# Kernel tuning notes

Hardware: AMD Instinct MI355X
Metric: run time of the kernel (lower is better)

Reference implementation:

```python
import jax, jax.numpy as jnp
import numpy as np
from jax import lax

B, N, S = 4, 16384, 4096
D1, D2 = 128, 256
MLP = (256, 128)
EPS_W = 1e-8
EPS_BN = 1e-5
BIG = 1e8


def setup_inputs() -> dict:
    key = jax.random.key(0)
    ks = jax.random.split(key, 10)
    inp = {
        "xyz1": jax.random.normal(ks[0], (B, 3, N), jnp.float32),
        "xyz2": jax.random.normal(ks[1], (B, 3, S), jnp.float32),
        "points1": jax.random.normal(ks[2], (B, D1, N), jnp.float32),
        "points2": jax.random.normal(ks[3], (B, D2, S), jnp.float32),
        "idx1": jnp.repeat(jnp.arange(B, dtype=jnp.int32), N).reshape(B, N),
        "idx2": jnp.repeat(jnp.arange(B, dtype=jnp.int32), S).reshape(B, S),
    }
    cin = D1 + D2
    inp["w1"] = jax.random.normal(ks[4], (MLP[0], cin), jnp.float32) * 0.05
    inp["b1"] = jnp.zeros((MLP[0],), jnp.float32)
    inp["g1"] = jnp.ones((MLP[0],), jnp.float32)
    inp["be1"] = jnp.zeros((MLP[0],), jnp.float32)
    inp["w2"] = jax.random.normal(ks[5], (MLP[1], MLP[0]), jnp.float32) * 0.05
    inp["b2"] = jnp.zeros((MLP[1],), jnp.float32)
    inp["g2"] = jnp.ones((MLP[1],), jnp.float32)
    inp["be2"] = jnp.zeros((MLP[1],), jnp.float32)
    return inp


def _bn_relu(x, gamma, beta):
    # training-mode batchnorm over (B, N) per channel, then relu; x: [B, C, N]
    mean = jnp.mean(x, axis=(0, 2), keepdims=True)
    var = jnp.var(x, axis=(0, 2), keepdims=True)  # biased, as torch BN
    xn = (x - mean) * lax.rsqrt(var + EPS_BN)
    return jax.nn.relu(xn * gamma[None, :, None] + beta[None, :, None])


def _fp_forward(xyz1, xyz2, points1, points2, idx1, idx2,
                w1, b1, g1, be1, w2, b2, g2, be2):
    x1 = jnp.transpose(xyz1, (0, 2, 1))  # [B, N, 3]
    x2 = jnp.transpose(xyz2, (0, 2, 1))  # [B, S, 3]
    p2 = jnp.transpose(points2, (0, 2, 1))  # [B, S, D2]

    # squared pairwise distances [B, N, S]
    d = -2.0 * jnp.einsum('bnc,bsc->bns', x1, x2)
    d = d + jnp.sum(x1 * x1, -1)[:, :, None] + jnp.sum(x2 * x2, -1)[:, None, :]
    d = jnp.where(idx1[:, :, None] == idx2[:, None, :], d, jnp.inf)

    # 3 nearest neighbors (top-k on negated distances == sort-ascending take 3)
    neg_d3, idx3 = lax.top_k(-d, 3)          # [B, N, 3]
    d3 = -neg_d3
    recip = 1.0 / (d3 + EPS_W)
    weight = recip / jnp.sum(recip, axis=2, keepdims=True)
    weight = jnp.where(d3 > BIG, 0.0, weight)
    weight = jnp.nan_to_num(weight)

    gathered = jax.vmap(lambda p, i: p[i])(p2, idx3)   # [B, N, 3, D2]
    interp = jnp.sum(gathered * weight[..., None], axis=2)  # [B, N, D2]

    newp = jnp.concatenate([jnp.transpose(points1, (0, 2, 1)), interp], axis=-1)
    newp = jnp.transpose(newp, (0, 2, 1))  # [B, D1+D2, N]

    # 1x1 conv -> BN -> relu, twice
    h = jnp.einsum('bcn,oc->bon', newp, w1) + b1[None, :, None]
    h = _bn_relu(h, g1, be1)
    h = jnp.einsum('bcn,oc->bon', h, w2) + b2[None, :, None]
    h = _bn_relu(h, g2, be2)
    return h


def reference(xyz1, xyz2, points1, points2, idx1, idx2,
              w1, b1, g1, be1, w2, b2, g2, be2):
    return _fp_forward(xyz1, xyz2, points1, points2, idx1, idx2,
                       w1, b1, g1, be1, w2, b2, g2, be2)
```

## Files before the change

### kernel.cpp

```cpp
#include <hip/hip_runtime.h>
#include <hip/hip_bf16.h>

#define INF_F (__builtin_inff())

typedef __attribute__((ext_vector_type(8))) short bf16x8;
typedef __attribute__((ext_vector_type(4))) float f32x4;

__device__ __forceinline__ unsigned short f2bf(float f) {
  __hip_bfloat16 h = __float2bfloat16(f);
  return __builtin_bit_cast(unsigned short, h);
}
__device__ __forceinline__ float bf2f(unsigned short u) {
  return __uint_as_float((unsigned)u << 16);
}

#define TOP3_INS(d, sj, E0, E1, E2, J0, J1, J2)                      \
  {                                                                  \
    bool l0 = (d) < E0, l1 = (d) < E1;                               \
    E2 = l1 ? E1 : (d); J2 = l1 ? J1 : (sj);                         \
    E1 = l0 ? E0 : (l1 ? (d) : E1); J1 = l0 ? J0 : (l1 ? (sj) : J1); \
    E0 = l0 ? (d) : E0; J0 = l0 ? (sj) : J0;                         \
  }


__global__ __launch_bounds__(256) void transpose_k(const float* __restrict__ in,
                                                   unsigned short* __restrict__ out) {
  __shared__ float tile[32][33];
  int b = blockIdx.z;
  int s0 = blockIdx.x * 32;
  int k0 = blockIdx.y * 32;
  int tx = threadIdx.x, ty = threadIdx.y;
  const float* src = in + ((size_t)b * 256 + k0) * 4096 + s0;
  for (int r = ty; r < 32; r += 8) tile[r][tx] = src[(size_t)r * 4096 + tx];
  __syncthreads();
  unsigned short* dst = out + ((size_t)b * 4096 + s0) * 256 + k0;
  for (int r = ty; r < 32; r += 8) dst[(size_t)r * 256 + tx] = f2bf(tile[tx][r]);
}

__global__ __launch_bounds__(256) void p1t_k(const float* __restrict__ p1,
                                             unsigned short* __restrict__ X) {
  __shared__ float tile[32][33];
  int b = blockIdx.z;
  int n0 = blockIdx.x * 32;
  int c0 = blockIdx.y * 32;
  int tx = threadIdx.x, ty = threadIdx.y;
  const float* src = p1 + ((size_t)b * 128 + c0) * 16384 + n0;
  for (int r = ty; r < 32; r += 8) tile[r][tx] = src[(size_t)r * 16384 + tx];
  __syncthreads();
  for (int r = ty; r < 32; r += 8)
    X[((size_t)(b * 16384 + n0 + r)) * 384 + c0 + tx] = f2bf(tile[tx][r]);
}

__global__ __launch_bounds__(256) void wcvt_k(const float* __restrict__ w1,
                                              const float* __restrict__ w2,
                                              unsigned short* __restrict__ w1b,
                                              unsigned short* __restrict__ w2b) {
  int id = blockIdx.x * 256 + threadIdx.x;
  if (id < 98304) w1b[id] = f2bf(w1[id]);
  else w2b[id - 98304] = f2bf(w2[id - 98304]);
}

__global__ __launch_bounds__(256) void knn_k(const float* __restrict__ xyz1,
                                             const float* __restrict__ xyz2,
                                             const int* __restrict__ idx1,
                                             const int* __restrict__ idx2,
                                             float* __restrict__ rec) {
  __shared__ float4 sP[256];
  int bid = blockIdx.x;
  int chunk = bid >> 4, sl = bid & 15;
  int b = chunk >> 4;
  int nloc = (chunk & 15) << 10;
  int t = threadIdx.x;
  int common = idx1[b * 16384 + nloc];
  int sbase = sl << 8;
  {
    int gs = sbase + t;
    float x = xyz2[(b * 3 + 0) * 4096 + gs];
    float y = xyz2[(b * 3 + 1) * 4096 + gs];
    float z = xyz2[(b * 3 + 2) * 4096 + gs];
    float w = fmaf(x, x, fmaf(y, y, z * z));
    int sid = idx2[b * 4096 + gs];
    w = (sid == common) ? w : 3e38f;
    sP[t] = make_float4(x, y, z, w);
  }
  __syncthreads();
  int q0i = b * 16384 + nloc + t;
  float px0 = xyz1[(b * 3 + 0) * 16384 + nloc + t];
  float py0 = xyz1[(b * 3 + 1) * 16384 + nloc + t];
  float pz0 = xyz1[(b * 3 + 2) * 16384 + nloc + t];
  float px1 = xyz1[(b * 3 + 0) * 16384 + nloc + t + 256];
  float py1 = xyz1[(b * 3 + 1) * 16384 + nloc + t + 256];
  float pz1 = xyz1[(b * 3 + 2) * 16384 + nloc + t + 256];
  float px2 = xyz1[(b * 3 + 0) * 16384 + nloc + t + 512];
  float py2 = xyz1[(b * 3 + 1) * 16384 + nloc + t + 512];
  float pz2 = xyz1[(b * 3 + 2) * 16384 + nloc + t + 512];
  float px3 = xyz1[(b * 3 + 0) * 16384 + nloc + t + 768];
  float py3 = xyz1[(b * 3 + 1) * 16384 + nloc + t + 768];
  float pz3 = xyz1[(b * 3 + 2) * 16384 + nloc + t + 768];
  int id0 = idx1[q0i], id1 = idx1[q0i + 256], id2 = idx1[q0i + 512], id3 = idx1[q0i + 768];
  float pn0 = fmaf(px0, px0, fmaf(py0, py0, pz0 * pz0));
  float pn1 = fmaf(px1, px1, fmaf(py1, py1, pz1 * pz1));
  float pn2 = fmaf(px2, px2, fmaf(py2, py2, pz2 * pz2));
  float pn3 = fmaf(px3, px3, fmaf(py3, py3, pz3 * pz3));
  float e00 = INF_F, e10 = INF_F, e20 = INF_F;
  float e01 = INF_F, e11 = INF_F, e21 = INF_F;
  float e02 = INF_F, e12 = INF_F, e22 = INF_F;
  float e03 = INF_F, e13 = INF_F, e23 = INF_F;
  int j00 = 0, j10 = 0, j20 = 0;
  int j01 = 0, j11 = 0, j21 = 0;
  int j02 = 0, j12 = 0, j22 = 0;
  int j03 = 0, j13 = 0, j23 = 0;
#pragma unroll 2
  for (int s = 0; s < 256; ++s) {
    float4 p = sP[s];
    int sj = sbase + s;
    float d0 = fmaf(-2.f, fmaf(px0, p.x, fmaf(py0, p.y, pz0 * p.z)), pn0 + p.w);
    float d1 = fmaf(-2.f, fmaf(px1, p.x, fmaf(py1, p.y, pz1 * p.z)), pn1 + p.w);
    float d2 = fmaf(-2.f, fmaf(px2, p.x, fmaf(py2, p.y, pz2 * p.z)), pn2 + p.w);
    float d3 = fmaf(-2.f, fmaf(px3, p.x, fmaf(py3, p.y, pz3 * p.z)), pn3 + p.w);
    if (d0 < e20) TOP3_INS(d0, sj, e00, e10, e20, j00, j10, j20);
    if (d1 < e21) TOP3_INS(d1, sj, e01, e11, e21, j01, j11, j21);
    if (d2 < e22) TOP3_INS(d2, sj, e02, e12, e22, j02, j12, j22);
    if (d3 < e23) TOP3_INS(d3, sj, e03, e13, e23, j03, j13, j23);
  }
#define KNN_FB(MYID, PX, PY, PZ, PN, E0, E1, E2, J0, J1, J2)              \
  if (__builtin_expect((MYID) != common, 0)) {                            \
    E0 = INF_F; E1 = INF_F; E2 = INF_F; J0 = 0; J1 = 0; J2 = 0;           \
    for (int s = 0; s < 256; ++s) {                                       \
      int gs = sbase + s;                                                 \
      float x = xyz2[(b * 3 + 0) * 4096 + gs];                            \
      float y = xyz2[(b * 3 + 1) * 4096 + gs];                            \
      float z = xyz2[(b * 3 + 2) * 4096 + gs];                            \
      float w = fmaf(x, x, fmaf(y, y, z * z));                            \
      float d = fmaf(-2.f, fmaf(PX, x, fmaf(PY, y, (PZ) * z)), (PN) + w); \
      d = (idx2[b * 4096 + gs] == (MYID)) ? d : INF_F;                    \
      if (d < E2) TOP3_INS(d, gs, E0, E1, E2, J0, J1, J2);                \
    }                                                                     \
  }
  KNN_FB(id0, px0, py0, pz0, pn0, e00, e10, e20, j00, j10, j20);
  KNN_FB(id1, px1, py1, pz1, pn1, e01, e11, e21, j01, j11, j21);
  KNN_FB(id2, px2, py2, pz2, pn2, e02, e12, e22, j02, j12, j22);
  KNN_FB(id3, px3, py3, pz3, pn3, e03, e13, e23, j03, j13, j23);
#undef KNN_FB
  {
    float* r = &rec[((size_t)sl * 65536 + q0i) * 6];
    r[0] = e00; r[1] = e10; r[2] = e20;
    ((int*)r)[3] = j00; ((int*)r)[4] = j10; ((int*)r)[5] = j20;
    r = &rec[((size_t)sl * 65536 + q0i + 256) * 6];
    r[0] = e01; r[1] = e11; r[2] = e21;
    ((int*)r)[3] = j01; ((int*)r)[4] = j11; ((int*)r)[5] = j21;
    r = &rec[((size_t)sl * 65536 + q0i + 512) * 6];
    r[0] = e02; r[1] = e12; r[2] = e22;
    ((int*)r)[3] = j02; ((int*)r)[4] = j12; ((int*)r)[5] = j22;
    r = &rec[((size_t)sl * 65536 + q0i + 768) * 6];
    r[0] = e03; r[1] = e13; r[2] = e23;
    ((int*)r)[3] = j03; ((int*)r)[4] = j13; ((int*)r)[5] = j23;
  }
}

__global__ __launch_bounds__(256) void knnmerge_k(const float* __restrict__ rec,
                                                  int* __restrict__ idx3,
                                                  float* __restrict__ wgt) {
  int i = blockIdx.x * 256 + threadIdx.x;
  float e0, e1, e2;
  int j0, j1, j2;
  {
    const float* r = &rec[(size_t)i * 6];
    e0 = r[0]; e1 = r[1]; e2 = r[2];
    j0 = ((const int*)r)[3]; j1 = ((const int*)r)[4]; j2 = ((const int*)r)[5];
  }
  for (int c = 1; c < 16; ++c) {
    const float* r = &rec[((size_t)c * 65536 + i) * 6];
    const int* ir = (const int*)r;
#pragma unroll
    for (int w = 0; w < 3; ++w) {
      float d = r[w];
      int sj = ir[3 + w];
      bool l0 = (d < e0) || (d == e0 && sj < j0);
      bool l1 = (d < e1) || (d == e1 && sj < j1);
      bool l2 = (d < e2) || (d == e2 && sj < j2);
      e2 = l1 ? e1 : (l2 ? d : e2);
      j2 = l1 ? j1 : (l2 ? sj : j2);
      e1 = l0 ? e0 : (l1 ? d : e1);
      j1 = l0 ? j0 : (l1 ? sj : j1);
      e0 = l0 ? d : e0;
      j0 = l0 ? sj : j0;
    }
  }
  float r0 = 1.f / (e0 + 1e-8f);
  float r1 = 1.f / (e1 + 1e-8f);
  float r2 = 1.f / (e2 + 1e-8f);
  float rs = r0 + r1 + r2;
  float w0 = (e0 > 1e8f) ? 0.f : r0 / rs;
  float w1 = (e1 > 1e8f) ? 0.f : r1 / rs;
  float w2 = (e2 > 1e8f) ? 0.f : r2 / rs;
  idx3[(size_t)i * 3 + 0] = j0; idx3[(size_t)i * 3 + 1] = j1; idx3[(size_t)i * 3 + 2] = j2;
  wgt[(size_t)i * 3 + 0] = w0;  wgt[(size_t)i * 3 + 1] = w1;  wgt[(size_t)i * 3 + 2] = w2;
}

__global__ __launch_bounds__(256) void interp_k(const unsigned short* __restrict__ p2t,
                                                const int* __restrict__ idx3,
                                                const float* __restrict__ wgt,
                                                unsigned short* __restrict__ X) {
  int i0 = blockIdx.x * 128;
  int b = i0 >> 14;
  int k = threadIdx.x;
  const unsigned short* base = p2t + (size_t)b * 4096 * 256;
#pragma unroll 2
  for (int ii = 0; ii < 128; ++ii) {
    int i = i0 + ii;
    int id0 = idx3[i * 3 + 0], id1 = idx3[i * 3 + 1], id2 = idx3[i * 3 + 2];
    float w0 = wgt[i * 3 + 0], w1v = wgt[i * 3 + 1], w2v = wgt[i * 3 + 2];
    float v = w0 * bf2f(base[id0 * 256 + k]);
    v = fmaf(w1v, bf2f(base[id1 * 256 + k]), v);
    v = fmaf(w2v, bf2f(base[id2 * 256 + k]), v);
    X[(size_t)i * 384 + 128 + k] = f2bf(v);
  }
}

__global__ __launch_bounds__(256) void gemm1_k(const unsigned short* __restrict__ X,
                                               const unsigned short* __restrict__ Wb,
                                               unsigned short* __restrict__ h1T) {
  __shared__ unsigned short sW[128][40];
  __shared__ unsigned short sX[128][40];
  int t = threadIdx.x;
  int i0 = blockIdx.x * 128;
  int c0 = blockIdx.y * 128;
  int w = t >> 6, lane = t & 63;
  int wc = (w & 1) * 64, wn = (w >> 1) * 64;
  int l15 = lane & 15, g = lane >> 4;
  f32x4 acc[4][4];
#pragma unroll
  for (int a = 0; a < 4; ++a)
#pragma unroll
    for (int bq = 0; bq < 4; ++bq) acc[a][bq] = (f32x4)0.f;
  int sr = t & 127, sh = t >> 7;
  for (int kc = 0; kc < 12; ++kc) {
    int k0 = kc * 32;
    __syncthreads();
    {
      const uint4* gw = (const uint4*)&Wb[(size_t)(c0 + sr) * 384 + k0 + sh * 16];
      uint4 v0 = gw[0], v1 = gw[1];
      *(uint4*)&sW[sr][sh * 16] = v0;
      *(uint4*)&sW[sr][sh * 16 + 8] = v1;
      const uint4* gx = (const uint4*)&X[(size_t)(i0 + sr) * 384 + k0 + sh * 16];
      uint4 x0 = gx[0], x1 = gx[1];
      *(uint4*)&sX[sr][sh * 16] = x0;
      *(uint4*)&sX[sr][sh * 16 + 8] = x1;
    }
    __syncthreads();
    bf16x8 a[4], b[4];
#pragma unroll
    for (int tm = 0; tm < 4; ++tm)
      a[tm] = *(const bf16x8*)&sW[wc + tm * 16 + l15][g * 8];
#pragma unroll
    for (int tn = 0; tn < 4; ++tn)
      b[tn] = *(const bf16x8*)&sX[wn + tn * 16 + l15][g * 8];
#pragma unroll
    for (int tm = 0; tm < 4; ++tm)
#pragma unroll
      for (int tn = 0; tn < 4; ++tn)
        acc[tm][tn] = __builtin_amdgcn_mfma_f32_16x16x32_bf16(a[tm], b[tn], acc[tm][tn], 0, 0, 0);
  }
#pragma unroll
  for (int tm = 0; tm < 4; ++tm)
#pragma unroll
    for (int tn = 0; tn < 4; ++tn) {
      int c = c0 + wc + tm * 16 + g * 4;
      int n = i0 + wn + tn * 16 + l15;
      f32x4 v = acc[tm][tn];
      ushort4 o;
      o.x = f2bf(v[0]); o.y = f2bf(v[1]); o.z = f2bf(v[2]); o.w = f2bf(v[3]);
      *(ushort4*)&h1T[(size_t)n * 256 + c] = o;
    }
}

__global__ __launch_bounds__(256) void bnstats1_k(const unsigned short* __restrict__ h,
                                                  float* __restrict__ part) {
  int t = threadIdx.x, q = t & 63, ro = t >> 6;
  int r0 = blockIdx.x * 256;
  float s0 = 0, s1 = 0, s2 = 0, s3 = 0, q0 = 0, q1 = 0, q2 = 0, q3 = 0;
  for (int it = 0; it < 64; ++it) {
    size_t r = r0 + it * 4 + ro;
    ushort4 v = *(const ushort4*)&h[r * 256 + q * 4];
    float f0 = bf2f(v.x), f1 = bf2f(v.y), f2 = bf2f(v.z), f3 = bf2f(v.w);
    s0 += f0; q0 += f0 * f0;
    s1 += f1; q1 += f1 * f1;
    s2 += f2; q2 += f2 * f2;
    s3 += f3; q3 += f3 * f3;
  }
  __shared__ float sm[256][8];
  sm[t][0] = s0; sm[t][1] = s1; sm[t][2] = s2; sm[t][3] = s3;
  sm[t][4] = q0; sm[t][5] = q1; sm[t][6] = q2; sm[t][7] = q3;
  __syncthreads();
  if (t < 64) {
#pragma unroll
    for (int j = 1; j < 4; ++j)
#pragma unroll
      for (int e = 0; e < 8; ++e) sm[t][e] += sm[t + 64 * j][e];
#pragma unroll
    for (int i = 0; i < 4; ++i) {
      part[((size_t)blockIdx.x * 256 + t * 4 + i) * 2 + 0] = sm[t][i];
      part[((size_t)blockIdx.x * 256 + t * 4 + i) * 2 + 1] = sm[t][4 + i];
    }
  }
}

__global__ __launch_bounds__(256) void bnstats2_k(const float* __restrict__ o2,
                                                  float* __restrict__ part) {
  int t = threadIdx.x, q = t & 31, ro = t >> 5;
  int r0 = blockIdx.x * 256;
  float s0 = 0, s1 = 0, s2 = 0, s3 = 0, q0 = 0, q1 = 0, q2 = 0, q3 = 0;
  for (int it = 0; it < 32; ++it) {
    size_t r = r0 + it * 8 + ro;
    float4 v = *(const float4*)&o2[r * 128 + q * 4];
    s0 += v.x; q0 += v.x * v.x;
    s1 += v.y; q1 += v.y * v.y;
    s2 += v.z; q2 += v.z * v.z;
    s3 += v.w; q3 += v.w * v.w;
  }
  __shared__ float sm[256][8];
  sm[t][0] = s0; sm[t][1] = s1; sm[t][2] = s2; sm[t][3] = s3;
  sm[t][4] = q0; sm[t][5] = q1; sm[t][6] = q2; sm[t][7] = q3;
  __syncthreads();
  if (t < 32) {
#pragma unroll
    for (int j = 1; j < 8; ++j)
#pragma unroll
      for (int e = 0; e < 8; ++e) sm[t][e] += sm[t + 32 * j][e];
#pragma unroll
    for (int i = 0; i < 4; ++i) {
      part[((size_t)blockIdx.x * 128 + t * 4 + i) * 2 + 0] = sm[t][i];
      part[((size_t)blockIdx.x * 128 + t * 4 + i) * 2 + 1] = sm[t][4 + i];
    }
  }
}

template <int C>
__global__ __launch_bounds__(256) void bnfold_k(const float* __restrict__ part,
                                                const float* __restrict__ g,
                                                const float* __restrict__ be,
                                                float* __restrict__ A,
                                                float* __restrict__ Cc) {
  int c = threadIdx.x;
  if (c >= C) return;
  float s1 = 0.f, s2 = 0.f;
  for (int b = 0; b < 256; ++b) {
    s1 += part[((size_t)b * C + c) * 2 + 0];
    s2 += part[((size_t)b * C + c) * 2 + 1];
  }
  float mean = s1 * (1.f / 65536.f);
  float var = s2 * (1.f / 65536.f) - mean * mean;
  float a = g[c] * rsqrtf(var + 1e-5f);
  A[c] = a;
  Cc[c] = be[c] - mean * a;
}

__global__ __launch_bounds__(256) void gemm2_k(const unsigned short* __restrict__ h1T,
                                               const unsigned short* __restrict__ Wb,
                                               const float* __restrict__ A,
                                               const float* __restrict__ C,
                                               float* __restrict__ o2) {
  __shared__ unsigned short sW[128][40];
  __shared__ unsigned short sX[128][40];
  int t = threadIdx.x;
  int i0 = blockIdx.x * 128;
  int w = t >> 6, lane = t & 63;
  int wc = (w & 1) * 64, wn = (w >> 1) * 64;
  int l15 = lane & 15, g = lane >> 4;
  f32x4 acc[4][4];
#pragma unroll
  for (int a = 0; a < 4; ++a)
#pragma unroll
    for (int bq = 0; bq < 4; ++bq) acc[a][bq] = (f32x4)0.f;
  int sr = t & 127, sh = t >> 7;
  for (int kc = 0; kc < 8; ++kc) {
    int k0 = kc * 32;
    int kcol = k0 + sh * 16;
    __syncthreads();
    {
      const uint4* gw = (const uint4*)&Wb[(size_t)sr * 256 + kcol];
      uint4 v0 = gw[0], v1 = gw[1];
      *(uint4*)&sW[sr][sh * 16] = v0;
      *(uint4*)&sW[sr][sh * 16 + 8] = v1;
      const uint4* gx = (const uint4*)&h1T[(size_t)(i0 + sr) * 256 + kcol];
      uint4 x0 = gx[0], x1 = gx[1];
      unsigned rr[8] = {x0.x, x0.y, x0.z, x0.w, x1.x, x1.y, x1.z, x1.w};
      unsigned ww[8];
#pragma unroll
      for (int e = 0; e < 8; ++e) {
        int ch = kcol + 2 * e;
        float f0 = bf2f((unsigned short)(rr[e] & 0xFFFFu));
        float f1 = bf2f((unsigned short)(rr[e] >> 16));
        f0 = fmaxf(fmaf(A[ch], f0, C[ch]), 0.f);
        f1 = fmaxf(fmaf(A[ch + 1], f1, C[ch + 1]), 0.f);
        ww[e] = (unsigned)f2bf(f0) | ((unsigned)f2bf(f1) << 16);
      }
      uint4 y0 = {ww[0], ww[1], ww[2], ww[3]};
      uint4 y1 = {ww[4], ww[5], ww[6], ww[7]};
      *(uint4*)&sX[sr][sh * 16] = y0;
      *(uint4*)&sX[sr][sh * 16 + 8] = y1;
    }
    __syncthreads();
    bf16x8 a[4], b[4];
#pragma unroll
    for (int tm = 0; tm < 4; ++tm)
      a[tm] = *(const bf16x8*)&sW[wc + tm * 16 + l15][g * 8];
#pragma unroll
    for (int tn = 0; tn < 4; ++tn)
      b[tn] = *(const bf16x8*)&sX[wn + tn * 16 + l15][g * 8];
#pragma unroll
    for (int tm = 0; tm < 4; ++tm)
#pragma unroll
      for (int tn = 0; tn < 4; ++tn)
        acc[tm][tn] = __builtin_amdgcn_mfma_f32_16x16x32_bf16(a[tm], b[tn], acc[tm][tn], 0, 0, 0);
  }
#pragma unroll
  for (int tm = 0; tm < 4; ++tm)
#pragma unroll
    for (int tn = 0; tn < 4; ++tn) {
      int c = wc + tm * 16 + g * 4;
      int n = i0 + wn + tn * 16 + l15;
      f32x4 v = acc[tm][tn];
      *(float4*)&o2[(size_t)n * 128 + c] = make_float4(v[0], v[1], v[2], v[3]);
    }
}

__global__ __launch_bounds__(256) void final_k(const float* __restrict__ o2,
                                               const float* __restrict__ A,
                                               const float* __restrict__ C,
                                               float* __restrict__ out) {
  __shared__ float tile[32][33];
  int b = blockIdx.z;
  int n0 = blockIdx.x * 32;
  int c0 = blockIdx.y * 32;
  int tx = threadIdx.x, ty = threadIdx.y;
  float a = A[c0 + tx], cc = C[c0 + tx];
  for (int r = ty; r < 32; r += 8) {
    float v = o2[(size_t)(b * 16384 + n0 + r) * 128 + c0 + tx];
    tile[r][tx] = fmaxf(fmaf(a, v, cc), 0.f);
  }
  __syncthreads();
  for (int r = ty; r < 32; r += 8)
    out[((size_t)(b * 128 + c0 + r)) * 16384 + n0 + tx] = tile[tx][r];
}

extern "C" void kernel_launch(void* const* d_in, const int* in_sizes, int n_in,
                              void* d_out, int out_size, void* d_ws, size_t ws_size,
                              hipStream_t stream) {
  const float* xyz1 = (const float*)d_in[0];
  const float* xyz2 = (const float*)d_in[1];
  const float* p1   = (const float*)d_in[2];
  const float* p2   = (const float*)d_in[3];
  const int*   idx1 = (const int*)d_in[4];
  const int*   idx2 = (const int*)d_in[5];
  const float* w1   = (const float*)d_in[6];
  const float* g1   = (const float*)d_in[8];
  const float* be1  = (const float*)d_in[9];
  const float* w2   = (const float*)d_in[10];
  const float* g2   = (const float*)d_in[12];
  const float* be2  = (const float*)d_in[13];
  float* out = (float*)d_out;

  char* ws = (char*)d_ws;
  int*            idx3 = (int*)(ws + 0x0);
  float*          wgt  = (float*)(ws + 0xC0000);
  unsigned short* X    = (unsigned short*)(ws + 0x180000);
  unsigned short* h1T  = (unsigned short*)(ws + 0x3180000);
  unsigned short* p2t  = (unsigned short*)(ws + 0x3180000);
  float*          o2   = (float*)(ws + 0x5180000);
  float*          rec  = (float*)(ws + 0x5180000);
  unsigned short* w1b  = (unsigned short*)(ws + 0x7180000);
  unsigned short* w2b  = (unsigned short*)(ws + 0x71B0000);
  float*          part1 = (float*)(ws + 0x71C0000);
  float*          part2 = (float*)(ws + 0x7240000);
  float*          a1   = (float*)(ws + 0x7280000);
  float*          c1   = a1 + 256;
  float*          a2   = c1 + 256;
  float*          c2   = a2 + 128;

  hipLaunchKernelGGL(transpose_k, dim3(128, 8, 4), dim3(32, 8), 0, stream, p2, p2t);
  hipLaunchKernelGGL(wcvt_k, dim3(512), dim3(256), 0, stream, w1, w2, w1b, w2b);
  hipLaunchKernelGGL(p1t_k, dim3(512, 4, 4), dim3(32, 8), 0, stream, p1, X);
  hipLaunchKernelGGL(knn_k, dim3(1024), dim3(256), 0, stream,
                     xyz1, xyz2, idx1, idx2, rec);
  hipLaunchKernelGGL(knnmerge_k, dim3(256), dim3(256), 0, stream, rec, idx3, wgt);
  hipLaunchKernelGGL(interp_k, dim3(512), dim3(256), 0, stream, p2t, idx3, wgt, X);
  hipLaunchKernelGGL(gemm1_k, dim3(512, 2), dim3(256), 0, stream, X, w1b, h1T);
  hipLaunchKernelGGL(bnstats1_k, dim3(256), dim3(256), 0, stream, h1T, part1);
  hipLaunchKernelGGL((bnfold_k<256>), dim3(1), dim3(256), 0, stream, part1, g1, be1, a1, c1);
  hipLaunchKernelGGL(gemm2_k, dim3(512), dim3(256), 0, stream, h1T, w2b, a1, c1, o2);
  hipLaunchKernelGGL(bnstats2_k, dim3(256), dim3(256), 0, stream, o2, part2);
  hipLaunchKernelGGL((bnfold_k<128>), dim3(1), dim3(256), 0, stream, part2, g2, be2, a2, c2);
  hipLaunchKernelGGL(final_k, dim3(512, 4, 4), dim3(32, 8), 0, stream, o2, a2, c2, out);
}
```

Measured before the change: 274.2 us.

## Repartition KNN: one query per thread over 1024-candidate slices with prepacked xyz2

A new pack_k kernel precomputes float4 (x,y,z,|p|^2 masked) for every xyz2 point once, so KNN blocks no longer rebuild shared tiles. knn_k now has each thread handle one query over 1024 candidates read directly from global memory (uniform across the wave, so cached/broadcast), instead of four queries over 256 candidates. This cuts the split partitions from 16 to 4, which shrinks the rec buffer and the merge work. The trade-off is less register-level reuse of each candidate load across queries, and an extra small kernel launch.

```diff
diff --git a/kernel.cpp b/kernel.cpp
--- a/kernel.cpp
+++ b/kernel.cpp
@@ -60,102 +60,70 @@
   else w2b[id - 98304] = f2bf(w2[id - 98304]);
 }
 
+__global__ __launch_bounds__(256) void pack_k(const float* __restrict__ xyz2,
+                                              const int* __restrict__ idx1,
+                                              const int* __restrict__ idx2,
+                                              float4* __restrict__ pack) {
+  int b = blockIdx.y;
+  int s = blockIdx.x * 256 + threadIdx.x;
+  float x = xyz2[(b * 3 + 0) * 4096 + s];
+  float y = xyz2[(b * 3 + 1) * 4096 + s];
+  float z = xyz2[(b * 3 + 2) * 4096 + s];
+  float w = fmaf(x, x, fmaf(y, y, z * z));
+  int common = idx1[b * 16384];
+  w = (idx2[b * 4096 + s] == common) ? w : 3e38f;
+  pack[b * 4096 + s] = make_float4(x, y, z, w);
+}
+
 __global__ __launch_bounds__(256) void knn_k(const float* __restrict__ xyz1,
                                              const float* __restrict__ xyz2,
                                              const int* __restrict__ idx1,
                                              const int* __restrict__ idx2,
+                                             const float4* __restrict__ pack,
                                              float* __restrict__ rec) {
-  __shared__ float4 sP[256];
   int bid = blockIdx.x;
-  int chunk = bid >> 4, sl = bid & 15;
-  int b = chunk >> 4;
-  int nloc = (chunk & 15) << 10;
+  int qg = bid >> 2, sl = bid & 3;
+  int b = qg >> 6;
+  int nloc = (qg & 63) << 8;
   int t = threadIdx.x;
-  int common = idx1[b * 16384 + nloc];
-  int sbase = sl << 8;
-  {
-    int gs = sbase + t;
-    float x = xyz2[(b * 3 + 0) * 4096 + gs];
-    float y = xyz2[(b * 3 + 1) * 4096 + gs];
-    float z = xyz2[(b * 3 + 2) * 4096 + gs];
-    float w = fmaf(x, x, fmaf(y, y, z * z));
-    int sid = idx2[b * 4096 + gs];
-    w = (sid == common) ? w : 3e38f;
-    sP[t] = make_float4(x, y, z, w);
-  }
-  __syncthreads();
-  int q0i = b * 16384 + nloc + t;
-  float px0 = xyz1[(b * 3 + 0) * 16384 + nloc + t];
-  float py0 = xyz1[(b * 3 + 1) * 16384 + nloc + t];
-  float pz0 = xyz1[(b * 3 + 2) * 16384 + nloc + t];
-  float px1 = xyz1[(b * 3 + 0) * 16384 + nloc + t + 256];
-  float py1 = xyz1[(b * 3 + 1) * 16384 + nloc + t + 256];
-  float pz1 = xyz1[(b * 3 + 2) * 16384 + nloc + t + 256];
-  float px2 = xyz1[(b * 3 + 0) * 16384 + nloc + t + 512];
-  float py2 = xyz1[(b * 3 + 1) * 16384 + nloc + t + 512];
-  float pz2 = xyz1[(b * 3 + 2) * 16384 + nloc + t + 512];
-  float px3 = xyz1[(b * 3 + 0) * 16384 + nloc + t + 768];
-  float py3 = xyz1[(b * 3 + 1) * 16384 + nloc + t + 768];
-  float pz3 = xyz1[(b * 3 + 2) * 16384 + nloc + t + 768];
-  int id0 = idx1[q0i], id1 = idx1[q0i + 256], id2 = idx1[q0i + 512], id3 = idx1[q0i + 768];
-  float pn0 = fmaf(px0, px0, fmaf(py0, py0, pz0 * pz0));
-  float pn1 = fmaf(px1, px1, fmaf(py1, py1, pz1 * pz1));
-  float pn2 = fmaf(px2, px2, fmaf(py2, py2, pz2 * pz2));
-  float pn3 = fmaf(px3, px3, fmaf(py3, py3, pz3 * pz3));
-  float e00 = INF_F, e10 = INF_F, e20 = INF_F;
-  float e01 = INF_F, e11 = INF_F, e21 = INF_F;
-  float e02 = INF_F, e12 = INF_F, e22 = INF_F;
-  float e03 = INF_F, e13 = INF_F, e23 = INF_F;
-  int j00 = 0, j10 = 0, j20 = 0;
-  int j01 = 0, j11 = 0, j21 = 0;
-  int j02 = 0, j12 = 0, j22 = 0;
-  int j03 = 0, j13 = 0, j23 = 0;
-#pragma unroll 2
-  for (int s = 0; s < 256; ++s) {
-    float4 p = sP[s];
-    int sj = sbase + s;
-    float d0 = fmaf(-2.f, fmaf(px0, p.x, fmaf(py0, p.y, pz0 * p.z)), pn0 + p.w);
-    float d1 = fmaf(-2.f, fmaf(px1, p.x, fmaf(py1, p.y, pz1 * p.z)), pn1 + p.w);
-    float d2 = fmaf(-2.f, fmaf(px2, p.x, fmaf(py2, p.y, pz2 * p.z)), pn2 + p.w);
-    float d3 = fmaf(-2.f, fmaf(px3, p.x, fmaf(py3, p.y, pz3 * p.z)), pn3 + p.w);
-    if (d0 < e20) TOP3_INS(d0, sj, e00, e10, e20, j00, j10, j20);
-    if (d1 < e21) TOP3_INS(d1, sj, e01, e11, e21, j01, j11, j21);
-    if (d2 < e22) TOP3_INS(d2, sj, e02, e12, e22, j02, j12, j22);
-    if (d3 < e23) TOP3_INS(d3, sj, e03, e13, e23, j03, j13, j23);
-  }
-#define KNN_FB(MYID, PX, PY, PZ, PN, E0, E1, E2, J0, J1, J2)              \
-  if (__builtin_expect((MYID) != common, 0)) {                            \
-    E0 = INF_F; E1 = INF_F; E2 = INF_F; J0 = 0; J1 = 0; J2 = 0;           \
-    for (int s = 0; s < 256; ++s) {                                       \
-      int gs = sbase + s;                                                 \
-      float x = xyz2[(b * 3 + 0) * 4096 + gs];                            \
-      float y = xyz2[(b * 3 + 1) * 4096 + gs];                            \
-      float z = xyz2[(b * 3 + 2) * 4096 + gs];                            \
-      float w = fmaf(x, x, fmaf(y, y, z * z));                            \
-      float d = fmaf(-2.f, fmaf(PX, x, fmaf(PY, y, (PZ) * z)), (PN) + w); \
-      d = (idx2[b * 4096 + gs] == (MYID)) ? d : INF_F;                    \
-      if (d < E2) TOP3_INS(d, gs, E0, E1, E2, J0, J1, J2);                \
-    }                                                                     \
-  }
-  KNN_FB(id0, px0, py0, pz0, pn0, e00, e10, e20, j00, j10, j20);
-  KNN_FB(id1, px1, py1, pz1, pn1, e01, e11, e21, j01, j11, j21);
-  KNN_FB(id2, px2, py2, pz2, pn2, e02, e12, e22, j02, j12, j22);
-  KNN_FB(id3, px3, py3, pz3, pn3, e03, e13, e23, j03, j13, j23);
-#undef KNN_FB
-  {
-    float* r = &rec[((size_t)sl * 65536 + q0i) * 6];
-    r[0] = e00; r[1] = e10; r[2] = e20;
-    ((int*)r)[3] = j00; ((int*)r)[4] = j10; ((int*)r)[5] = j20;
-    r = &rec[((size_t)sl * 65536 + q0i + 256) * 6];
-    r[0] = e01; r[1] = e11; r[2] = e21;
-    ((int*)r)[3] = j01; ((int*)r)[4] = j11; ((int*)r)[5] = j21;
-    r = &rec[((size_t)sl * 65536 + q0i + 512) * 6];
-    r[0] = e02; r[1] = e12; r[2] = e22;
-    ((int*)r)[3] = j02; ((int*)r)[4] = j12; ((int*)r)[5] = j22;
-    r = &rec[((size_t)sl * 65536 + q0i + 768) * 6];
-    r[0] = e03; r[1] = e13; r[2] = e23;
-    ((int*)r)[3] = j03; ((int*)r)[4] = j13; ((int*)r)[5] = j23;
-  }
+  int n = nloc + t;
+  int q0i = b * 16384 + n;
+  int common = idx1[b * 16384];
+  int sbase = sl << 10;
+  const float4* ps = pack + b * 4096 + sbase;
+  float px = xyz1[(b * 3 + 0) * 16384 + n];
+  float py = xyz1[(b * 3 + 1) * 16384 + n];
+  float pz = xyz1[(b * 3 + 2) * 16384 + n];
+  int myid = idx1[q0i];
+  float pn = fmaf(px, px, fmaf(py, py, pz * pz));
+  float qx = -2.f * px, qy = -2.f * py, qz = -2.f * pz;
+  float e0 = INF_F, e1 = INF_F, e2 = INF_F;
+  int j0 = 0, j1 = 0, j2 = 0;
+#pragma unroll 8
+  for (int s = 0; s < 1024; ++s) {
+    float4 p = ps[s];
+    float d = fmaf(qx, p.x, fmaf(qy, p.y, fmaf(qz, p.z, pn))) + p.w;
+    if (__builtin_expect(d < e2, 0)) {
+      int sj = sbase + s;
+      TOP3_INS(d, sj, e0, e1, e2, j0, j1, j2);
+    }
+  }
+  if (__builtin_expect(myid != common, 0)) {
+    e0 = INF_F; e1 = INF_F; e2 = INF_F; j0 = 0; j1 = 0; j2 = 0;
+    for (int s = 0; s < 1024; ++s) {
+      int gs = sbase + s;
+      float x = xyz2[(b * 3 + 0) * 4096 + gs];
+      float y = xyz2[(b * 3 + 1) * 4096 + gs];
+      float z = xyz2[(b * 3 + 2) * 4096 + gs];
+      float w = fmaf(x, x, fmaf(y, y, z * z));
+      float d = fmaf(qx, x, fmaf(qy, y, fmaf(qz, z, pn))) + w;
+      d = (idx2[b * 4096 + gs] == myid) ? d : INF_F;
+      if (d < e2) TOP3_INS(d, gs, e0, e1, e2, j0, j1, j2);
+    }
+  }
+  float* r = &rec[((size_t)sl * 65536 + q0i) * 6];
+  r[0] = e0; r[1] = e1; r[2] = e2;
+  ((int*)r)[3] = j0; ((int*)r)[4] = j1; ((int*)r)[5] = j2;
 }
 
 __global__ __launch_bounds__(256) void knnmerge_k(const float* __restrict__ rec,
@@ -169,7 +137,8 @@
     e0 = r[0]; e1 = r[1]; e2 = r[2];
     j0 = ((const int*)r)[3]; j1 = ((const int*)r)[4]; j2 = ((const int*)r)[5];
   }
-  for (int c = 1; c < 16; ++c) {
+#pragma unroll
+  for (int c = 1; c < 4; ++c) {
     const float* r = &rec[((size_t)c * 65536 + i) * 6];
     const int* ir = (const int*)r;
 #pragma unroll
@@ -474,7 +443,8 @@
   unsigned short* w2b  = (unsigned short*)(ws + 0x71B0000);
   float*          part1 = (float*)(ws + 0x71C0000);
   float*          part2 = (float*)(ws + 0x7240000);
-  float*          a1   = (float*)(ws + 0x7280000);
+  float4*         pack = (float4*)(ws + 0x7280000);
+  float*          a1   = (float*)(ws + 0x72C8000);
   float*          c1   = a1 + 256;
   float*          a2   = c1 + 256;
   float*          c2   = a2 + 128;
@@ -482,8 +452,9 @@
   hipLaunchKernelGGL(transpose_k, dim3(128, 8, 4), dim3(32, 8), 0, stream, p2, p2t);
   hipLaunchKernelGGL(wcvt_k, dim3(512), dim3(256), 0, stream, w1, w2, w1b, w2b);
   hipLaunchKernelGGL(p1t_k, dim3(512, 4, 4), dim3(32, 8), 0, stream, p1, X);
+  hipLaunchKernelGGL(pack_k, dim3(16, 4), dim3(256), 0, stream, xyz2, idx1, idx2, pack);
   hipLaunchKernelGGL(knn_k, dim3(1024), dim3(256), 0, stream,
-                     xyz1, xyz2, idx1, idx2, rec);
+                     xyz1, xyz2, idx1, idx2, pack, rec);
   hipLaunchKernelGGL(knnmerge_k, dim3(256), dim3(256), 0, stream, rec, idx3, wgt);
   hipLaunchKernelGGL(interp_k, dim3(512), dim3(256), 0, stream, p2t, idx3, wgt, X);
   hipLaunchKernelGGL(gemm1_k, dim3(512, 2), dim3(256), 0, stream, X, w1b, h1T);
```

Measured after the change: 276.3 us. Within noise of the previous version (+0.8%).
